# Performance work log

Hardware: AMD Instinct MI355X
Metric: run time of the kernel (lower is better)

The kernel has to match this reference:

```python
import jax, jax.numpy as jnp
import numpy as np

MAX_REL_POS = 16


def relative_position_ids(t, max_pos):
    r = jnp.arange(t)
    dist = jnp.clip(r[None, :] - r[:, None], -max_pos, max_pos)
    return dist + max_pos  # [T, T] in [0, 2*max_pos]


def setup_inputs():
    key = jax.random.key(0)
    ks = jax.random.split(key, 5)
    B, H, T, D = 2, 16, 1024, 64
    V = 2 * MAX_REL_POS + 1  # 33
    q = jax.random.normal(ks[0], (B, H, T, D), dtype=jnp.float32)
    k = jax.random.normal(ks[1], (B, H, T, D), dtype=jnp.float32)
    v = jax.random.normal(ks[2], (B, H, T, D), dtype=jnp.float32)
    embed_k = jax.random.normal(ks[3], (V, D), dtype=jnp.float32)
    embed_v = jax.random.normal(ks[4], (V, D), dtype=jnp.float32)
    mask = jnp.zeros((1, 1, T, T), dtype=jnp.float32)
    return {"q": q, "k": k, "v": v, "embed_k": embed_k, "embed_v": embed_v, "mask": mask}


def reference(q, k, v, embed_k, embed_v, mask):
    T = q.shape[2]
    D = k.shape[-1]
    rel = relative_position_ids(T, MAX_REL_POS)           # [T, T] int
    rel_k = embed_k[rel]                                   # [T, T, D]
    rel_v = embed_v[rel]                                   # [T, T, D]
    # QK^T plus relative-key term (matmul_with_relative_representations, transpose_b=True)
    logits = jnp.einsum('bhqd,bhkd->bhqk', q, k) + jnp.einsum('bhqd,qkd->bhqk', q, rel_k)
    logits = logits * (1.0 / jnp.sqrt(jnp.asarray(D, dtype=logits.dtype)))
    logits = logits + mask * (-1e9)
    attn = jax.nn.softmax(logits, axis=-1)                 # [B, H, T, T]
    out = jnp.einsum('bhqk,bhkd->bhqd', attn, v) + jnp.einsum('bhqk,qkd->bhqd', attn, rel_v)
    return out, attn
```

## Files before the change

kernel.cpp:

```cpp
#include <hip/hip_runtime.h>

#define BHN 32
#define T 1024
#define DD 64
#define TQ 16

typedef __attribute__((ext_vector_type(8))) __bf16 bf16x8;
typedef __attribute__((ext_vector_type(8))) unsigned short us8;
typedef __attribute__((ext_vector_type(4))) float f32x4;

struct alignas(16) U4 { unsigned a, b, c, d; };

__device__ __forceinline__ unsigned short f2bf(float x) {
  unsigned u = __builtin_bit_cast(unsigned, x);
  u += 0x7fffu + ((u >> 16) & 1u);
  return (unsigned short)(u >> 16);
}
__device__ __forceinline__ float bf2f(unsigned short h) {
  unsigned u = ((unsigned)h) << 16;
  return __builtin_bit_cast(float, u);
}
__device__ __forceinline__ bf16x8 ld_bf16x8(const unsigned short* p) {
  U4 u = *(const U4*)p;
  return __builtin_bit_cast(bf16x8, u);
}

__global__ __launch_bounds__(256) void prep_conv(
    const float* __restrict__ k, const float* __restrict__ v,
    unsigned short* __restrict__ kbf, unsigned short* __restrict__ vt)
{
  __shared__ float sT[64][65];
  const int bh = blockIdx.y;
  const int tb = blockIdx.x * 64;
  const int t = threadIdx.x;
  const size_t base = (size_t)bh * T * DD + (size_t)tb * DD;

  const float4* ksrc = (const float4*)(k + base);
  ushort4* kdst = (ushort4*)(kbf + base);
#pragma unroll
  for (int i = 0; i < 4; ++i) {
    int g = i * 256 + t;
    float4 f = ksrc[g];
    ushort4 u;
    u.x = f2bf(f.x); u.y = f2bf(f.y); u.z = f2bf(f.z); u.w = f2bf(f.w);
    kdst[g] = u;
  }

  const float* vsrc = v + base;
#pragma unroll
  for (int i = 0; i < 16; ++i) {
    int e = i * 256 + t;
    sT[e & 63][e >> 6] = vsrc[e];
  }
  __syncthreads();
  unsigned short* vdst = vt + (size_t)bh * DD * T + tb;
#pragma unroll
  for (int i = 0; i < 16; ++i) {
    int e = i * 256 + t;
    int dd = e >> 6, kk = e & 63;
    vdst[(size_t)dd * T + kk] = f2bf(sT[dd][kk]);
  }
}

__global__ __launch_bounds__(256, 6) void attn_main(
    const float* __restrict__ q, const unsigned short* __restrict__ kbf,
    const unsigned short* __restrict__ vt, const float* __restrict__ ek,
    const float* __restrict__ ev, const float* __restrict__ mask,
    float* __restrict__ out, float* __restrict__ attn)
{
  __shared__ float sQek[TQ][33];
  __shared__ float sDiag[TQ][31];
  __shared__ float sRS[4][TQ];
  __shared__ float sRB[4][TQ];
  __shared__ float sInv[TQ];
  __shared__ float sB0n[TQ];
  __shared__ alignas(16) unsigned short sTile[4][16][40];
  __shared__ float sOr[4][TQ][66];

  const int bh = blockIdx.y;
  const int qb = blockIdx.x * TQ;
  const int tid = threadIdx.x;
  const int wave = tid >> 6;
  const int lane = tid & 63;
  const int quad = lane >> 4;
  const int col = lane & 15;

  for (int i = tid; i < TQ * 31; i += 256) (&sDiag[0][0])[i] = 0.f;

  const float* qrows = q + (size_t)bh * T * DD + (size_t)qb * DD;
  for (int idx = tid; idx < TQ * 33; idx += 256) {
    int i = idx / 33;
    int r = idx - i * 33;
    const float4* qa = (const float4*)(qrows + i * DD);
    const float4* eb = (const float4*)(ek + r * DD);
    float acc = 0.f;
#pragma unroll
    for (int d4 = 0; d4 < 16; ++d4) {
      float4 a = qa[d4], b = eb[d4];
      acc += a.x * b.x + a.y * b.y + a.z * b.z + a.w * b.w;
    }
    sQek[i][r] = acc;
  }
  __syncthreads();

  bf16x8 aq0, aq1;
  {
    const float* qp = qrows + col * DD + quad * 8;
    float4 f0 = *(const float4*)(qp);
    float4 f1 = *(const float4*)(qp + 4);
    float4 f2 = *(const float4*)(qp + 32);
    float4 f3 = *(const float4*)(qp + 36);
    us8 u0, u1;
    u0[0] = f2bf(f0.x); u0[1] = f2bf(f0.y); u0[2] = f2bf(f0.z); u0[3] = f2bf(f0.w);
    u0[4] = f2bf(f1.x); u0[5] = f2bf(f1.y); u0[6] = f2bf(f1.z); u0[7] = f2bf(f1.w);
    u1[0] = f2bf(f2.x); u1[1] = f2bf(f2.y); u1[2] = f2bf(f2.z); u1[3] = f2bf(f2.w);
    u1[4] = f2bf(f3.x); u1[5] = f2bf(f3.y); u1[6] = f2bf(f3.z); u1[7] = f2bf(f3.w);
    aq0 = __builtin_bit_cast(bf16x8, u0);
    aq1 = __builtin_bit_cast(bf16x8, u1);
  }

  float regS[4] = {0.f, 0.f, 0.f, 0.f};
  float regB[4] = {0.f, 0.f, 0.f, 0.f};
  const unsigned short* kbh = kbf + (size_t)bh * T * DD;
  for (int it = 0; it < 16; ++it) {
    int kt = wave * 256 + it * 16;
    int kg = kt + col;
    const unsigned short* kp = kbh + (size_t)kg * DD + quad * 8;
    bf16x8 bk0 = ld_bf16x8(kp);
    bf16x8 bk1 = ld_bf16x8(kp + 32);
    f32x4 acc = {0.f, 0.f, 0.f, 0.f};
    acc = __builtin_amdgcn_mfma_f32_16x16x32_bf16(aq0, bk0, acc, 0, 0, 0);
    acc = __builtin_amdgcn_mfma_f32_16x16x32_bf16(aq1, bk1, acc, 0, 0, 0);
#pragma unroll
    for (int r = 0; r < 4; ++r) {
      int row = quad * 4 + r;
      int qg = qb + row;
      int dk = kg - qg;
      int rel = dk < -16 ? 0 : (dk > 16 ? 32 : dk + 16);
      float logit = (acc[r] + sQek[row][rel]) * 0.125f
                  + mask[(size_t)qg * T + kg] * (-1e9f);
      float p = __expf(fminf(logit, 80.f));
      regS[r] += p;
      if (dk <= -16) regB[r] += p;
      if ((unsigned)(dk + 15) < 31u) sDiag[row][dk + 15] = p;
    }
  }

#pragma unroll
  for (int r = 0; r < 4; ++r) {
    float s = regS[r], b = regB[r];
#pragma unroll
    for (int off = 1; off < 16; off <<= 1) {
      s += __shfl_xor(s, off, 64);
      b += __shfl_xor(b, off, 64);
    }
    if (col == 0) { sRS[wave][quad * 4 + r] = s; sRB[wave][quad * 4 + r] = b; }
  }
  __syncthreads();
  if (tid < TQ) {
    float S = sRS[0][tid] + sRS[1][tid] + sRS[2][tid] + sRS[3][tid];
    float B0 = sRB[0][tid] + sRB[1][tid] + sRB[2][tid] + sRB[3][tid];
    float inv = 1.f / S;
    sInv[tid] = inv;
    sB0n[tid] = B0 * inv;
  }
  __syncthreads();

  float invr[4];
#pragma unroll
  for (int r = 0; r < 4; ++r) invr[r] = sInv[quad * 4 + r];

  float* attnq = attn + (size_t)bh * T * T + (size_t)qb * T;
  const unsigned short* vtb = vt + (size_t)bh * DD * T;
  f32x4 zero4 = {0.f, 0.f, 0.f, 0.f};
  f32x4 oacc[4];
#pragma unroll
  for (int dt = 0; dt < 4; ++dt) oacc[dt] = zero4;

  for (int c = 0; c < 8; ++c) {
#pragma unroll
    for (int sub = 0; sub < 2; ++sub) {
      const int it = c * 2 + sub;
      const int kt = wave * 256 + it * 16;
      const int kg = kt + col;
      const unsigned short* kp = kbh + (size_t)kg * DD + quad * 8;
      bf16x8 bk0 = ld_bf16x8(kp);
      bf16x8 bk1 = ld_bf16x8(kp + 32);
      f32x4 acc = {0.f, 0.f, 0.f, 0.f};
      acc = __builtin_amdgcn_mfma_f32_16x16x32_bf16(aq0, bk0, acc, 0, 0, 0);
      acc = __builtin_amdgcn_mfma_f32_16x16x32_bf16(aq1, bk1, acc, 0, 0, 0);
#pragma unroll
      for (int r = 0; r < 4; ++r) {
        int row = quad * 4 + r;
        int qg = qb + row;
        int dk = kg - qg;
        int rel = dk < -16 ? 0 : (dk > 16 ? 32 : dk + 16);
        float logit = (acc[r] + sQek[row][rel]) * 0.125f
                    + mask[(size_t)qg * T + kg] * (-1e9f);
        float p = __expf(fminf(logit, 80.f));
        __builtin_nontemporal_store(p * invr[r], attnq + (size_t)row * T + kg);
        sTile[wave][row][sub * 16 + col] = f2bf(p);
      }
    }
    bf16x8 ap = ld_bf16x8(&sTile[wave][col][quad * 8]);
    const unsigned short* vp = vtb + (size_t)col * T + (wave * 256 + c * 32 + quad * 8);
#pragma unroll
    for (int dt = 0; dt < 4; ++dt) {
      bf16x8 bv = ld_bf16x8(vp + (size_t)(dt * 16) * T);
      oacc[dt] = __builtin_amdgcn_mfma_f32_16x16x32_bf16(ap, bv, oacc[dt], 0, 0, 0);
    }
  }

#pragma unroll
  for (int dt = 0; dt < 4; ++dt)
#pragma unroll
    for (int r = 0; r < 4; ++r)
      sOr[wave][quad * 4 + r][dt * 16 + col] = oacc[dt][r];
  __syncthreads();

  const int d = tid & 63;
  float ev0 = ev[d];
  float ev32 = ev[32 * DD + d];
  float accv[4], invq[4], sd[4];
#pragma unroll
  for (int r = 0; r < 4; ++r) {
    int row = wave * 4 + r;
    float o = sOr[0][row][d] + sOr[1][row][d] + sOr[2][row][d] + sOr[3][row][d];
    float inv = sInv[row];
    invq[r] = inv;
    float b0 = sB0n[row];
    accv[r] = o * inv + b0 * ev0 + (1.f - b0) * ev32;
    sd[r] = 0.f;
  }
  for (int j = 0; j < 31; ++j) {
    float e = ev[(j + 1) * DD + d];
#pragma unroll
    for (int r = 0; r < 4; ++r) {
      float pd = sDiag[wave * 4 + r][j];
      sd[r] += pd;
      accv[r] += pd * invq[r] * e;
    }
  }
  float* outp = out + (size_t)bh * T * DD + (size_t)qb * DD;
#pragma unroll
  for (int r = 0; r < 4; ++r)
    outp[(size_t)(wave * 4 + r) * DD + d] = accv[r] - sd[r] * invq[r] * ev32;
}

extern "C" void kernel_launch(void* const* d_in, const int* in_sizes, int n_in,
                              void* d_out, int out_size, void* d_ws, size_t ws_size,
                              hipStream_t stream) {
  const float* q    = (const float*)d_in[0];
  const float* k    = (const float*)d_in[1];
  const float* v    = (const float*)d_in[2];
  const float* ek   = (const float*)d_in[3];
  const float* ev   = (const float*)d_in[4];
  const float* mask = (const float*)d_in[5];

  float* out  = (float*)d_out;
  float* attn = out + (size_t)BHN * T * DD;

  unsigned short* kbf = (unsigned short*)d_ws;
  unsigned short* vt  = kbf + (size_t)BHN * T * DD;

  dim3 pg(T / 64, BHN);
  prep_conv<<<pg, 256, 0, stream>>>(k, v, kbf, vt);

  dim3 g(T / TQ, BHN);
  attn_main<<<g, 256, 0, stream>>>(q, kbf, vt, ek, ev, mask, out, attn);
}
```

Before: 314.5 us.

## Cache bf16 probabilities in registers instead of recomputing QK in second pass

The first pass now keeps the unnormalized probabilities, packed as bf16, in 32 registers per thread. The second pass reuses them for the attention writeback and the PV MFMA, so K is no longer reloaded and the QK MFMAs and exp are not recomputed. The MFMA operands are swapped so each lane owns one query row, which gives vectorized float4 mask loads and float4 attention stores. The cost is higher register pressure, with occupancy lowered from 6 to 4 blocks per SM. The written attn values are also now rounded through bf16 instead of kept in fp32, which lowers their precision.

```diff
diff --git a/kernel.cpp b/kernel.cpp
--- a/kernel.cpp
+++ b/kernel.cpp
@@ -23,6 +23,9 @@
 __device__ __forceinline__ bf16x8 ld_bf16x8(const unsigned short* p) {
   U4 u = *(const U4*)p;
   return __builtin_bit_cast(bf16x8, u);
+}
+__device__ __forceinline__ unsigned packbf(float a, float b) {
+  return (unsigned)f2bf(a) | ((unsigned)f2bf(b) << 16);
 }
 
 __global__ __launch_bounds__(256) void prep_conv(
@@ -62,7 +65,7 @@
   }
 }
 
-__global__ __launch_bounds__(256, 6) void attn_main(
+__global__ __launch_bounds__(256, 4) void attn_main(
     const float* __restrict__ q, const unsigned short* __restrict__ kbf,
     const unsigned short* __restrict__ vt, const float* __restrict__ ek,
     const float* __restrict__ ev, const float* __restrict__ mask,
@@ -119,43 +122,45 @@
     aq1 = __builtin_bit_cast(bf16x8, u1);
   }
 
-  float regS[4] = {0.f, 0.f, 0.f, 0.f};
-  float regB[4] = {0.f, 0.f, 0.f, 0.f};
+  const int wb = wave * 256;
+  const int qg = qb + col;
+  const float c0 = sQek[col][0], c32 = sQek[col][32];
   const unsigned short* kbh = kbf + (size_t)bh * T * DD;
+  const float* maskq = mask + (size_t)qg * T + wb;
+  unsigned w[32];
+  float regS = 0.f, regB = 0.f;
+#pragma unroll
   for (int it = 0; it < 16; ++it) {
-    int kt = wave * 256 + it * 16;
-    int kg = kt + col;
-    const unsigned short* kp = kbh + (size_t)kg * DD + quad * 8;
+    const int kt = wb + it * 16;
+    const unsigned short* kp = kbh + (size_t)(kt + col) * DD + quad * 8;
     bf16x8 bk0 = ld_bf16x8(kp);
     bf16x8 bk1 = ld_bf16x8(kp + 32);
+    float4 m4 = *(const float4*)(maskq + it * 16 + quad * 4);
     f32x4 acc = {0.f, 0.f, 0.f, 0.f};
-    acc = __builtin_amdgcn_mfma_f32_16x16x32_bf16(aq0, bk0, acc, 0, 0, 0);
-    acc = __builtin_amdgcn_mfma_f32_16x16x32_bf16(aq1, bk1, acc, 0, 0, 0);
+    acc = __builtin_amdgcn_mfma_f32_16x16x32_bf16(bk0, aq0, acc, 0, 0, 0);
+    acc = __builtin_amdgcn_mfma_f32_16x16x32_bf16(bk1, aq1, acc, 0, 0, 0);
+    float mv[4] = {m4.x, m4.y, m4.z, m4.w};
+    float p4[4];
 #pragma unroll
     for (int r = 0; r < 4; ++r) {
-      int row = quad * 4 + r;
-      int qg = qb + row;
+      int kg = kt + quad * 4 + r;
       int dk = kg - qg;
-      int rel = dk < -16 ? 0 : (dk > 16 ? 32 : dk + 16);
-      float logit = (acc[r] + sQek[row][rel]) * 0.125f
-                  + mask[(size_t)qg * T + kg] * (-1e9f);
+      float qv = dk < 0 ? c0 : c32;
+      if ((unsigned)(dk + 16) <= 32u) qv = sQek[col][dk + 16];
+      float logit = (acc[r] + qv) * 0.125f + mv[r] * (-1e9f);
       float p = __expf(fminf(logit, 80.f));
-      regS[r] += p;
-      if (dk <= -16) regB[r] += p;
-      if ((unsigned)(dk + 15) < 31u) sDiag[row][dk + 15] = p;
-    }
-  }
-
-#pragma unroll
-  for (int r = 0; r < 4; ++r) {
-    float s = regS[r], b = regB[r];
-#pragma unroll
-    for (int off = 1; off < 16; off <<= 1) {
-      s += __shfl_xor(s, off, 64);
-      b += __shfl_xor(b, off, 64);
-    }
-    if (col == 0) { sRS[wave][quad * 4 + r] = s; sRB[wave][quad * 4 + r] = b; }
-  }
+      p4[r] = p;
+      regS += p;
+      if (dk <= -16) regB += p;
+      if ((unsigned)(dk + 15) < 31u) sDiag[col][dk + 15] = p;
+    }
+    w[it * 2]     = packbf(p4[0], p4[1]);
+    w[it * 2 + 1] = packbf(p4[2], p4[3]);
+  }
+
+  regS += __shfl_xor(regS, 16, 64); regS += __shfl_xor(regS, 32, 64);
+  regB += __shfl_xor(regB, 16, 64); regB += __shfl_xor(regB, 32, 64);
+  if (quad == 0) { sRS[wave][col] = regS; sRB[wave][col] = regB; }
   __syncthreads();
   if (tid < TQ) {
     float S = sRS[0][tid] + sRS[1][tid] + sRS[2][tid] + sRS[3][tid];
@@ -166,47 +171,34 @@
   }
   __syncthreads();
 
-  float invr[4];
-#pragma unroll
-  for (int r = 0; r < 4; ++r) invr[r] = sInv[quad * 4 + r];
-
-  float* attnq = attn + (size_t)bh * T * T + (size_t)qb * T;
+  const float inv = sInv[col];
+  float* arow = attn + (size_t)bh * T * T + (size_t)qg * T + wb + quad * 4;
+#pragma unroll
+  for (int it = 0; it < 16; ++it) {
+    unsigned w0 = w[it * 2], w1 = w[it * 2 + 1];
+    float4 o;
+    o.x = bf2f((unsigned short)(w0 & 0xffffu)) * inv;
+    o.y = bf2f((unsigned short)(w0 >> 16)) * inv;
+    o.z = bf2f((unsigned short)(w1 & 0xffffu)) * inv;
+    o.w = bf2f((unsigned short)(w1 >> 16)) * inv;
+    *(float4*)(arow + it * 16) = o;
+  }
+
   const unsigned short* vtb = vt + (size_t)bh * DD * T;
-  f32x4 zero4 = {0.f, 0.f, 0.f, 0.f};
   f32x4 oacc[4];
 #pragma unroll
-  for (int dt = 0; dt < 4; ++dt) oacc[dt] = zero4;
-
+  for (int dt = 0; dt < 4; ++dt) { f32x4 z = {0.f,0.f,0.f,0.f}; oacc[dt] = z; }
+#pragma unroll
   for (int c = 0; c < 8; ++c) {
-#pragma unroll
-    for (int sub = 0; sub < 2; ++sub) {
-      const int it = c * 2 + sub;
-      const int kt = wave * 256 + it * 16;
-      const int kg = kt + col;
-      const unsigned short* kp = kbh + (size_t)kg * DD + quad * 8;
-      bf16x8 bk0 = ld_bf16x8(kp);
-      bf16x8 bk1 = ld_bf16x8(kp + 32);
-      f32x4 acc = {0.f, 0.f, 0.f, 0.f};
-      acc = __builtin_amdgcn_mfma_f32_16x16x32_bf16(aq0, bk0, acc, 0, 0, 0);
-      acc = __builtin_amdgcn_mfma_f32_16x16x32_bf16(aq1, bk1, acc, 0, 0, 0);
-#pragma unroll
-      for (int r = 0; r < 4; ++r) {
-        int row = quad * 4 + r;
-        int qg = qb + row;
-        int dk = kg - qg;
-        int rel = dk < -16 ? 0 : (dk > 16 ? 32 : dk + 16);
-        float logit = (acc[r] + sQek[row][rel]) * 0.125f
-                    + mask[(size_t)qg * T + kg] * (-1e9f);
-        float p = __expf(fminf(logit, 80.f));
-        __builtin_nontemporal_store(p * invr[r], attnq + (size_t)row * T + kg);
-        sTile[wave][row][sub * 16 + col] = f2bf(p);
-      }
-    }
+    *(unsigned*)&sTile[wave][col][quad * 4]          = w[c * 4 + 0];
+    *(unsigned*)&sTile[wave][col][quad * 4 + 2]      = w[c * 4 + 1];
+    *(unsigned*)&sTile[wave][col][16 + quad * 4]     = w[c * 4 + 2];
+    *(unsigned*)&sTile[wave][col][16 + quad * 4 + 2] = w[c * 4 + 3];
     bf16x8 ap = ld_bf16x8(&sTile[wave][col][quad * 8]);
-    const unsigned short* vp = vtb + (size_t)col * T + (wave * 256 + c * 32 + quad * 8);
 #pragma unroll
     for (int dt = 0; dt < 4; ++dt) {
-      bf16x8 bv = ld_bf16x8(vp + (size_t)(dt * 16) * T);
+      const unsigned short* vp = vtb + (size_t)(dt * 16 + col) * T + wb + c * 32 + quad * 8;
+      bf16x8 bv = ld_bf16x8(vp);
       oacc[dt] = __builtin_amdgcn_mfma_f32_16x16x32_bf16(ap, bv, oacc[dt], 0, 0, 0);
     }
   }
@@ -226,10 +218,10 @@
   for (int r = 0; r < 4; ++r) {
     int row = wave * 4 + r;
     float o = sOr[0][row][d] + sOr[1][row][d] + sOr[2][row][d] + sOr[3][row][d];
-    float inv = sInv[row];
-    invq[r] = inv;
+    float iv = sInv[row];
+    invq[r] = iv;
     float b0 = sB0n[row];
-    accv[r] = o * inv + b0 * ev0 + (1.f - b0) * ev32;
+    accv[r] = o * iv + b0 * ev0 + (1.f - b0) * ev32;
     sd[r] = 0.f;
   }
   for (int j = 0; j < 31; ++j) {
```

Measured after the change: 296.8 us. 1.06x faster.
